# Performance work log

Hardware: AMD Instinct MI355X
Metric: run time of the kernel (lower is better)

Reference implementation:

```python
import jax, jax.numpy as jnp
import numpy as np

D_MODEL, D_STATE, D_CONV, EXPAND = 1024, 16, 4, 2
D_INNER = EXPAND * D_MODEL
B, L = 2, 4096
LN_EPS = 1e-5


def setup_inputs() -> dict:
    key = jax.random.key(0)
    ks = jax.random.split(key, 6)
    x = jax.random.normal(ks[0], (B, L, D_MODEL), dtype=jnp.float32)
    ln_gamma = jnp.ones((D_MODEL,), jnp.float32)
    ln_beta = jnp.zeros((D_MODEL,), jnp.float32)
    W_in = jax.random.normal(ks[1], (2 * D_INNER, D_MODEL), jnp.float32) / np.sqrt(D_MODEL).astype(np.float32)
    conv_w = jax.random.normal(ks[2], (D_INNER, 1, D_CONV), jnp.float32) * 0.1
    conv_b = jnp.zeros((D_INNER,), jnp.float32)
    W_out = jax.random.normal(ks[3], (D_MODEL, D_INNER), jnp.float32) / np.sqrt(D_INNER).astype(np.float32)
    A = jnp.eye(D_STATE, dtype=jnp.float32)
    Bm = jax.random.normal(ks[4], (D_STATE, D_INNER), jnp.float32) * 0.01
    Cm = jax.random.normal(ks[5], (D_STATE, D_INNER), jnp.float32) * 0.01
    return dict(x=x, ln_gamma=ln_gamma, ln_beta=ln_beta, W_in=W_in,
                conv_w=conv_w, conv_b=conv_b, W_out=W_out, A=A, Bm=Bm, Cm=Cm)


def _layernorm(x, gamma, beta):
    mu = jnp.mean(x, axis=-1, keepdims=True)
    var = jnp.mean(jnp.square(x - mu), axis=-1, keepdims=True)
    return (x - mu) * jax.lax.rsqrt(var + LN_EPS) * gamma + beta


def _causal_depthwise_conv(xp, conv_w, conv_b):
    # xp: (B, L, D_INNER) -> torch Conv1d(padding=K-1, groups=C) then slice [:L]
    # == left-pad K-1, valid depthwise conv.
    lhs = jnp.pad(xp.transpose(0, 2, 1), ((0, 0), (0, 0), (D_CONV - 1, 0)))  # (B,C,L+K-1)
    out = jax.lax.conv_general_dilated(
        lhs, conv_w, window_strides=(1,), padding='VALID',
        dimension_numbers=('NCH', 'OIH', 'NCH'), feature_group_count=D_INNER)
    return out.transpose(0, 2, 1) + conv_b  # (B, L, C)


def reference(x, ln_gamma, ln_beta, W_in, conv_w, conv_b, W_out, A, Bm, Cm):
    # scan permutation is identity (untrained optimizer state); masking disabled
    xn = _layernorm(x, ln_gamma, ln_beta)
    xz = jnp.einsum('bld,ed->ble', xn, W_in)          # (B, L, 2*D_INNER)
    x_part, z = jnp.split(xz, 2, axis=-1)             # each (B, L, D_INNER)
    x_conv = jax.nn.silu(_causal_depthwise_conv(x_part, conv_w, conv_b))

    # recurrence: s_t = s_{t-1} @ A.T + u_t @ B.T ; out_t = (x_conv_t + s_t @ C) * sigmoid(z_t)
    u_seq = x_part.transpose(1, 0, 2)                 # (L, B, D_INNER)
    xc_seq = x_conv.transpose(1, 0, 2)
    z_seq = z.transpose(1, 0, 2)

    def step(state, inp):
        u_t, xc_t, z_t = inp
        state = state @ A.T + u_t @ Bm.T              # (B, D_STATE)
        out = (xc_t + state @ Cm) * jax.nn.sigmoid(z_t)
        return state, out

    state0 = jnp.zeros((x.shape[0], D_STATE), x.dtype)
    _, ys = jax.lax.scan(step, state0, (u_seq, xc_seq, z_seq))
    y = ys.transpose(1, 0, 2)                         # (B, L, D_INNER)
    residual = jnp.einsum('bli,di->bld', y, W_out)    # (B, L, D_MODEL)
    return x + residual
```

## Files before the change

kernel.cpp:

```cpp
#include <hip/hip_runtime.h>
#include <hip/hip_bf16.h>
#include <math.h>

#define D_MODEL 1024
#define D_STATE 16
#define D_CONV 4
#define D_INNER 2048
#define BATCH 2
#define SEQ 4096
#define NROW (BATCH * SEQ)
#define LN_EPS 1e-5f

typedef __attribute__((ext_vector_type(8))) short  bf16x8_t;
typedef __attribute__((ext_vector_type(4))) float  f32x4_t;
typedef __attribute__((ext_vector_type(8))) unsigned short u16x8_t;

__device__ inline unsigned short f2bf(float f) {
    unsigned u = __float_as_uint(f);
    u += 0x7fffu + ((u >> 16) & 1u);
    return (unsigned short)(u >> 16);
}
__device__ inline float bf2f(unsigned short u) {
    return __uint_as_float((unsigned)u << 16);
}

#define GLL16(g, l)                                                            \
    __builtin_amdgcn_global_load_lds(                                          \
        (const __attribute__((address_space(1))) void*)(g),                    \
        (__attribute__((address_space(3))) void*)(l), 16, 0, 0)

#define FENCE asm volatile("" ::: "memory")
#define BAR do { FENCE; __builtin_amdgcn_s_barrier(); FENCE; } while (0)

__global__ __launch_bounds__(256) void cvt_all(const float* __restrict__ W_in,
                                               const float* __restrict__ W_out,
                                               const float* __restrict__ Bm,
                                               unsigned short* __restrict__ Win_bf,
                                               unsigned short* __restrict__ Wout_bf,
                                               unsigned short* __restrict__ Bm_bf) {
    const long long g = (long long)(blockIdx.x * 256 + threadIdx.x) * 8;
    const long long n1 = (long long)2 * D_INNER * D_MODEL;
    const long long n2 = n1 + (long long)D_MODEL * D_INNER;
    const float* src; unsigned short* dst; long long off;
    if (g < n1)      { src = W_in;  dst = Win_bf;  off = g; }
    else if (g < n2) { src = W_out; dst = Wout_bf; off = g - n1; }
    else             { src = Bm;    dst = Bm_bf;   off = g - n2; }
    const float4 a = *reinterpret_cast<const float4*>(src + off);
    const float4 b = *reinterpret_cast<const float4*>(src + off + 4);
    u16x8_t p;
    p[0] = f2bf(a.x); p[1] = f2bf(a.y); p[2] = f2bf(a.z); p[3] = f2bf(a.w);
    p[4] = f2bf(b.x); p[5] = f2bf(b.y); p[6] = f2bf(b.z); p[7] = f2bf(b.w);
    *reinterpret_cast<u16x8_t*>(dst + off) = p;
}

__global__ __launch_bounds__(256) void ln_kernel(const float* __restrict__ x,
                                                 const float* __restrict__ gamma,
                                                 const float* __restrict__ beta,
                                                 unsigned short* __restrict__ xn) {
    const int row = blockIdx.x;
    const int tid = threadIdx.x;
    const float4* xr = reinterpret_cast<const float4*>(x + (size_t)row * D_MODEL);
    float4 v = xr[tid];

    __shared__ float red[8];
    const int lane = tid & 63, wave = tid >> 6;

    float s = v.x + v.y + v.z + v.w;
    #pragma unroll
    for (int off = 32; off > 0; off >>= 1) s += __shfl_down(s, off, 64);
    if (lane == 0) red[wave] = s;
    __syncthreads();
    float mu = (red[0] + red[1] + red[2] + red[3]) * (1.0f / D_MODEL);
    __syncthreads();

    float dx = v.x - mu, dy = v.y - mu, dz = v.z - mu, dw = v.w - mu;
    float ss = dx * dx + dy * dy + dz * dz + dw * dw;
    #pragma unroll
    for (int off = 32; off > 0; off >>= 1) ss += __shfl_down(ss, off, 64);
    if (lane == 0) red[wave] = ss;
    __syncthreads();
    float var = (red[0] + red[1] + red[2] + red[3]) * (1.0f / D_MODEL);
    float rs = rsqrtf(var + LN_EPS);

    const float4 gv = reinterpret_cast<const float4*>(gamma)[tid];
    const float4 bv = reinterpret_cast<const float4*>(beta)[tid];
    ushort4 o;
    o.x = f2bf(dx * rs * gv.x + bv.x);
    o.y = f2bf(dy * rs * gv.y + bv.y);
    o.z = f2bf(dz * rs * gv.z + bv.z);
    o.w = f2bf(dw * rs * gv.w + bv.w);
    reinterpret_cast<ushort4*>(xn + (size_t)row * D_MODEL)[tid] = o;
}

__global__ __launch_bounds__(512) void gemm256_bf16(const short* __restrict__ A,
                                                    const short* __restrict__ B,
                                                    unsigned short* __restrict__ Cb,
                                                    int M, int N, int K) {
    __shared__ short lds[2 * 4 * 8192];

    const int tid = threadIdx.x;
    const int w = tid >> 6, l = tid & 63;
    const int row0 = blockIdx.y * 256;
    const int col0 = blockIdx.x * 256;
    const int wm = w >> 2;
    const int wn = w & 3;
    const int fr = l & 15;
    const int fc = (l >> 4) * 8;
    const int NT = K >> 6;

    const int qa = wm;
    const int qb = 2 + (wn >> 1);
    const int bb = (wn & 1) * 64;

    auto STAGE = [&](const short* __restrict__ G, int growbase, int k0,
                     int buf, int q) {
        #pragma unroll
        for (int j = 0; j < 2; ++j) {
            const int e = ((j * 8 + w) << 9) + l * 8;
            const int r = e >> 6;
            const int c = (e & 63) ^ ((r & 7) << 3);
            GLL16(G + (size_t)(growbase + r) * K + k0 + c,
                  &lds[buf * 32768 + q * 8192 + ((j * 8 + w) << 9)]);
        }
    };
    auto LDF = [&](int buf, int q, int r, int ks) -> bf16x8_t {
        const int c = (ks * 32 + fc) ^ ((r & 7) << 3);
        return *reinterpret_cast<const bf16x8_t*>(
            &lds[buf * 32768 + q * 8192 + r * 64 + c]);
    };

    f32x4_t acc[8][4] = {};
    bf16x8_t af[4][2], bA[2][2], bB[2][2];

#define MFMA_Q(mh, nh, bfr)                                                    \
    do {                                                                       \
        _Pragma("unroll")                                                      \
        for (int mi = 0; mi < 4; ++mi)                                         \
            _Pragma("unroll")                                                  \
            for (int ni = 0; ni < 2; ++ni)                                     \
                _Pragma("unroll")                                              \
                for (int ks = 0; ks < 2; ++ks)                                 \
                    acc[(mh) * 4 + mi][(nh) * 2 + ni] =                        \
                        __builtin_amdgcn_mfma_f32_16x16x32_bf16(               \
                            af[mi][ks], bfr[ni][ks],                           \
                            acc[(mh) * 4 + mi][(nh) * 2 + ni], 0, 0, 0);       \
    } while (0)

    STAGE(A, row0,       0, 0, 0);
    STAGE(A, row0 + 128, 0, 0, 1);
    STAGE(B, col0,       0, 0, 2);
    STAGE(B, col0 + 128, 0, 0, 3);
    if (NT > 1) {
        STAGE(B, col0,       64, 1, 2);
        STAGE(B, col0 + 128, 64, 1, 3);
        STAGE(A, row0,       64, 1, 0);
        asm volatile("s_waitcnt vmcnt(6)" ::: "memory");
    } else {
        asm volatile("s_waitcnt vmcnt(0)" ::: "memory");
    }
    BAR;

    for (int kt = 0; kt < NT; ++kt) {
        const int buf = kt & 1, nbuf = buf ^ 1;
        #pragma unroll
        for (int mi = 0; mi < 4; ++mi)
            #pragma unroll
            for (int ks = 0; ks < 2; ++ks)
                af[mi][ks] = LDF(buf, qa, mi * 16 + fr, ks);
        #pragma unroll
        for (int ni = 0; ni < 2; ++ni)
            #pragma unroll
            for (int ks = 0; ks < 2; ++ks)
                bA[ni][ks] = LDF(buf, qb, bb + ni * 16 + fr, ks);
        if (kt + 1 < NT) STAGE(A, row0 + 128, (kt + 1) << 6, nbuf, 1);
        BAR;
        __builtin_amdgcn_s_setprio(1);
        MFMA_Q(0, 0, bA);
        __builtin_amdgcn_s_setprio(0);
        BAR;
        #pragma unroll
        for (int ni = 0; ni < 2; ++ni)
            #pragma unroll
            for (int ks = 0; ks < 2; ++ks)
                bB[ni][ks] = LDF(buf, qb, bb + 32 + ni * 16 + fr, ks);
        BAR;
        __builtin_amdgcn_s_setprio(1);
        MFMA_Q(0, 1, bB);
        __builtin_amdgcn_s_setprio(0);
        BAR;
        #pragma unroll
        for (int mi = 0; mi < 4; ++mi)
            #pragma unroll
            for (int ks = 0; ks < 2; ++ks)
                af[mi][ks] = LDF(buf, qa, 64 + mi * 16 + fr, ks);
        if (kt + 2 < NT) {
            STAGE(B, col0,       (kt + 2) << 6, buf, 2);
            STAGE(B, col0 + 128, (kt + 2) << 6, buf, 3);
        }
        BAR;
        __builtin_amdgcn_s_setprio(1);
        MFMA_Q(1, 1, bB);
        __builtin_amdgcn_s_setprio(0);
        BAR;
        if (kt + 2 < NT) {
            STAGE(A, row0, (kt + 2) << 6, buf, 0);
            asm volatile("s_waitcnt vmcnt(6)" ::: "memory");
        } else {
            asm volatile("s_waitcnt vmcnt(0)" ::: "memory");
        }
        BAR;
        __builtin_amdgcn_s_setprio(1);
        MFMA_Q(1, 0, bA);
        __builtin_amdgcn_s_setprio(0);
        BAR;
    }
#undef MFMA_Q

    const int cr = (l >> 4) * 4;
    const int cc = l & 15;
    #pragma unroll
    for (int m = 0; m < 8; ++m) {
        #pragma unroll
        for (int n = 0; n < 4; ++n) {
            size_t base = (size_t)(row0 + wm * 128 + m * 16 + cr) * N +
                          (col0 + wn * 64 + n * 16 + cc);
            #pragma unroll
            for (int j = 0; j < 4; ++j)
                Cb[base + (size_t)j * N] = f2bf(acc[m][n][j]);
        }
    }
}

__global__ __launch_bounds__(512) void gemm_out(const short* __restrict__ A,
                                                const short* __restrict__ B,
                                                const float* __restrict__ add,
                                                float* __restrict__ C,
                                                int M, int N, int K) {
    __shared__ short lds[2 * 3 * 8192];

    const int tid = threadIdx.x;
    const int w = tid >> 6, l = tid & 63;

    const int id = blockIdx.y * gridDim.x + blockIdx.x;
    const int cpx = (gridDim.x * gridDim.y) >> 3;
    const int sid = (id & 7) * cpx + (id >> 3);
    const int row0 = (sid / gridDim.x) * 256;
    const int col0 = (sid % gridDim.x) * 128;

    const int wm = w >> 2;
    const int wn = w & 3;
    const int fr = l & 15;
    const int fc = (l >> 4) * 8;
    const int NT = K >> 6;
    const int bb = wn * 32;

    auto STAGE = [&](const short* __restrict__ G, int growbase, int k0,
                     int buf, int q) {
        #pragma unroll
        for (int j = 0; j < 2; ++j) {
            const int e = ((j * 8 + w) << 9) + l * 8;
            const int r = e >> 6;
            const int c = (e & 63) ^ ((r & 7) << 3);
            GLL16(G + (size_t)(growbase + r) * K + k0 + c,
                  &lds[buf * 24576 + q * 8192 + ((j * 8 + w) << 9)]);
        }
    };
    auto LDF = [&](int buf, int q, int r, int ks) -> bf16x8_t {
        const int c = (ks * 32 + fc) ^ ((r & 7) << 3);
        return *reinterpret_cast<const bf16x8_t*>(
            &lds[buf * 24576 + q * 8192 + r * 64 + c]);
    };

    f32x4_t acc[8][2] = {};
    bf16x8_t af[4][2], bA[2], bB[2];

#define MFMA_H(mh, an, bfr)                                                    \
    do {                                                                       \
        _Pragma("unroll")                                                      \
        for (int mi = 0; mi < 4; ++mi)                                         \
            _Pragma("unroll")                                                  \
            for (int ks = 0; ks < 2; ++ks)                                     \
                acc[(mh) * 4 + mi][(an)] =                                     \
                    __builtin_amdgcn_mfma_f32_16x16x32_bf16(                   \
                        af[mi][ks], bfr[ks], acc[(mh) * 4 + mi][(an)], 0, 0, 0);\
    } while (0)

    STAGE(A, row0,       0, 0, 0);
    STAGE(A, row0 + 128, 0, 0, 1);
    STAGE(B, col0,       0, 0, 2);
    if (NT > 1) {
        STAGE(B, col0, 64, 1, 2);
        STAGE(A, row0, 64, 1, 0);
        asm volatile("s_waitcnt vmcnt(4)" ::: "memory");
    } else {
        asm volatile("s_waitcnt vmcnt(0)" ::: "memory");
    }
    BAR;

    for (int kt = 0; kt < NT; ++kt) {
        const int buf = kt & 1, nbuf = buf ^ 1;
        #pragma unroll
        for (int mi = 0; mi < 4; ++mi)
            #pragma unroll
            for (int ks = 0; ks < 2; ++ks)
                af[mi][ks] = LDF(buf, wm, mi * 16 + fr, ks);
        #pragma unroll
        for (int ks = 0; ks < 2; ++ks)
            bA[ks] = LDF(buf, 2, bb + fr, ks);
        if (kt + 1 < NT) STAGE(A, row0 + 128, (kt + 1) << 6, nbuf, 1);
        BAR;
        __builtin_amdgcn_s_setprio(1);
        MFMA_H(0, 0, bA);
        __builtin_amdgcn_s_setprio(0);
        BAR;
        #pragma unroll
        for (int ks = 0; ks < 2; ++ks)
            bB[ks] = LDF(buf, 2, bb + 16 + fr, ks);
        BAR;
        __builtin_amdgcn_s_setprio(1);
        MFMA_H(0, 1, bB);
        __builtin_amdgcn_s_setprio(0);
        BAR;
        #pragma unroll
        for (int mi = 0; mi < 4; ++mi)
            #pragma unroll
            for (int ks = 0; ks < 2; ++ks)
                af[mi][ks] = LDF(buf, wm, 64 + mi * 16 + fr, ks);
        if (kt + 2 < NT) STAGE(B, col0, (kt + 2) << 6, buf, 2);
        BAR;
        __builtin_amdgcn_s_setprio(1);
        MFMA_H(1, 1, bB);
        __builtin_amdgcn_s_setprio(0);
        BAR;
        if (kt + 2 < NT) {
            STAGE(A, row0, (kt + 2) << 6, buf, 0);
            asm volatile("s_waitcnt vmcnt(4)" ::: "memory");
        } else {
            asm volatile("s_waitcnt vmcnt(0)" ::: "memory");
        }
        BAR;
        __builtin_amdgcn_s_setprio(1);
        MFMA_H(1, 0, bA);
        __builtin_amdgcn_s_setprio(0);
        BAR;
    }
#undef MFMA_H

    const int cr = (l >> 4) * 4;
    const int cc = l & 15;
    #pragma unroll
    for (int m = 0; m < 8; ++m) {
        #pragma unroll
        for (int n = 0; n < 2; ++n) {
            size_t base = (size_t)(row0 + wm * 128 + m * 16 + cr) * N +
                          (col0 + wn * 32 + n * 16 + cc);
            #pragma unroll
            for (int j = 0; j < 4; ++j)
                C[base + (size_t)j * N] = acc[m][n][j] + add[base + (size_t)j * N];
        }
    }
}

__global__ __launch_bounds__(64) void v_mfma(const unsigned short* __restrict__ xz,
                                             const unsigned short* __restrict__ Bmb,
                                             float* __restrict__ V) {
    const int l = threadIdx.x;
    const int r0 = blockIdx.x * 16;
    const int fr = l & 15;
    const int fk = (l >> 4) * 8;

    const unsigned short* aP = xz + (size_t)(r0 + fr) * (2 * D_INNER) + fk;
    const unsigned short* bP = Bmb + fr * D_INNER + fk;

    f32x4_t acc = {};
    #pragma unroll 4
    for (int k0 = 0; k0 < D_INNER; k0 += 32) {
        bf16x8_t a = *reinterpret_cast<const bf16x8_t*>(aP + k0);
        bf16x8_t b = *reinterpret_cast<const bf16x8_t*>(bP + k0);
        acc = __builtin_amdgcn_mfma_f32_16x16x32_bf16(a, b, acc, 0, 0, 0);
    }

    const int cr = (l >> 4) * 4;
    const int cc = l & 15;
    #pragma unroll
    for (int j = 0; j < 4; ++j)
        V[(size_t)(r0 + cr + j) * D_STATE + cc] = acc[j];
}

__global__ __launch_bounds__(256) void check_a(const float* __restrict__ A,
                                               int* __restrict__ flag) {
    const int i = threadIdx.x;
    if (i == 0) *flag = 0;
    __syncthreads();
    const float ex = ((i >> 4) == (i & 15)) ? 1.0f : 0.0f;
    unsigned long long bad = __ballot(A[i] != ex);
    if ((i & 63) == 0 && bad) atomicOr(flag, 1);
}

__global__ __launch_bounds__(256) void scan_par(const float* __restrict__ V,
                                                float* __restrict__ S,
                                                const int* __restrict__ flag) {
    if (*flag) return;
    const int p = blockIdx.x;
    const int b = p >> 4, s = p & 15;
    const int tid = threadIdx.x;
    const float* vb = V + (size_t)b * SEQ * D_STATE + s;
    float* sb = S + (size_t)b * SEQ * D_STATE + s;

    const int t0 = tid * 16;
    float v[16];
    float run = 0.0f;
    #pragma unroll
    for (int j = 0; j < 16; ++j) {
        run += vb[(size_t)(t0 + j) * D_STATE];
        v[j] = run;
    }

    const float tot = run;
    float sc = tot;
    #pragma unroll
    for (int off = 1; off < 64; off <<= 1) {
        float n = __shfl_up(sc, off, 64);
        if ((tid & 63) >= off) sc += n;
    }
    __shared__ float wtot[4];
    if ((tid & 63) == 63) wtot[tid >> 6] = sc;
    __syncthreads();
    float woff = 0.0f;
    #pragma unroll
    for (int w2 = 0; w2 < 4; ++w2)
        if (w2 < (tid >> 6)) woff += wtot[w2];
    const float excl = sc - tot + woff;

    #pragma unroll
    for (int j = 0; j < 16; ++j)
        sb[(size_t)(t0 + j) * D_STATE] = v[j] + excl;
}

#define SCAN_CHUNK 256

__global__ __launch_bounds__(64) void scan_seq(const float* __restrict__ V,
                                               const float* __restrict__ A,
                                               float* __restrict__ S,
                                               const int* __restrict__ flag) {
    if (*flag == 0) return;
    __shared__ float Al[D_STATE * D_STATE];
    __shared__ float Vl[2 * SCAN_CHUNK * D_STATE];
    __shared__ float Sl[2 * SCAN_CHUNK * D_STATE];

    const int tid = threadIdx.x;
    for (int i = tid; i < D_STATE * D_STATE; i += 64) Al[i] = A[i];
    __syncthreads();

    float st = 0.0f;
    const int bb = (tid >> 4) & 1;
    const int ss = tid & 15;

    for (int t0 = 0; t0 < SEQ; t0 += SCAN_CHUNK) {
        for (int idx = tid; idx < 2 * SCAN_CHUNK * D_STATE; idx += 64) {
            int b = idx >> 12;
            int rem = idx & 4095;
            Vl[idx] = V[((size_t)(b * SEQ + t0) * D_STATE) + rem];
        }
        __syncthreads();

        if (tid < 32) {
            float* vb = Vl + bb * SCAN_CHUNK * D_STATE + ss;
            float* sb = Sl + bb * SCAN_CHUNK * D_STATE + ss;
            for (int t = 0; t < SCAN_CHUNK; ++t) {
                float ns = vb[t * D_STATE];
                #pragma unroll
                for (int s2 = 0; s2 < D_STATE; ++s2) {
                    float other = __shfl(st, (tid & 16) | s2, 64);
                    ns = fmaf(Al[ss * D_STATE + s2], other, ns);
                }
                st = ns;
                sb[t * D_STATE] = st;
            }
        }
        __syncthreads();

        for (int idx = tid; idx < 2 * SCAN_CHUNK * D_STATE; idx += 64) {
            int b = idx >> 12;
            int rem = idx & 4095;
            S[((size_t)(b * SEQ + t0) * D_STATE) + rem] = Sl[idx];
        }
        __syncthreads();
    }
}

__global__ __launch_bounds__(256) void y_kernel(const unsigned short* __restrict__ xz,
                                                const float* __restrict__ S,
                                                const float* __restrict__ Cm,
                                                const float* __restrict__ convw,
                                                const float* __restrict__ convb,
                                                unsigned short* __restrict__ y) {
    const int tid = threadIdx.x;
    const int i0 = blockIdx.x * 512 + tid * 2;
    const int r0 = blockIdx.y * 64;
    const int tb0 = r0 & (SEQ - 1);

    const float4 w0 = *reinterpret_cast<const float4*>(&convw[i0 * D_CONV]);
    const float4 w1 = *reinterpret_cast<const float4*>(&convw[(i0 + 1) * D_CONV]);
    const float cb0 = convb[i0], cb1 = convb[i0 + 1];
    float cm0[D_STATE], cm1[D_STATE];
    #pragma unroll
    for (int s = 0; s < D_STATE; ++s) {
        float2 c = *reinterpret_cast<const float2*>(&Cm[s * D_INNER + i0]);
        cm0[s] = c.x; cm1[s] = c.y;
    }

    float2 xm1 = make_float2(0.f, 0.f), xm2 = xm1, xm3 = xm1;
    if (tb0 >= 1) { ushort2 u = *reinterpret_cast<const ushort2*>(&xz[(size_t)(r0 - 1) * (2 * D_INNER) + i0]); xm1 = make_float2(bf2f(u.x), bf2f(u.y)); }
    if (tb0 >= 2) { ushort2 u = *reinterpret_cast<const ushort2*>(&xz[(size_t)(r0 - 2) * (2 * D_INNER) + i0]); xm2 = make_float2(bf2f(u.x), bf2f(u.y)); }
    if (tb0 >= 3) { ushort2 u = *reinterpret_cast<const ushort2*>(&xz[(size_t)(r0 - 3) * (2 * D_INNER) + i0]); xm3 = make_float2(bf2f(u.x), bf2f(u.y)); }

    for (int r = r0; r < r0 + 64; ++r) {
        const ushort2 xu = *reinterpret_cast<const ushort2*>(&xz[(size_t)r * (2 * D_INNER) + i0]);
        const ushort2 zu = *reinterpret_cast<const ushort2*>(&xz[(size_t)r * (2 * D_INNER) + D_INNER + i0]);
        const float2 x0 = make_float2(bf2f(xu.x), bf2f(xu.y));

        float a0 = cb0;
        a0 = fmaf(w0.x, xm3.x, a0); a0 = fmaf(w0.y, xm2.x, a0);
        a0 = fmaf(w0.z, xm1.x, a0); a0 = fmaf(w0.w, x0.x, a0);
        float a1 = cb1;
        a1 = fmaf(w1.x, xm3.y, a1); a1 = fmaf(w1.y, xm2.y, a1);
        a1 = fmaf(w1.z, xm1.y, a1); a1 = fmaf(w1.w, x0.y, a1);

        const float xc0 = a0 / (1.0f + expf(-a0));
        const float xc1 = a1 / (1.0f + expf(-a1));

        const float4* Sp = reinterpret_cast<const float4*>(S + (size_t)r * D_STATE);
        const float4 s0 = Sp[0], s1 = Sp[1], s2 = Sp[2], s3 = Sp[3];
        const float sv[D_STATE] = {s0.x, s0.y, s0.z, s0.w, s1.x, s1.y, s1.z, s1.w,
                                   s2.x, s2.y, s2.z, s2.w, s3.x, s3.y, s3.z, s3.w};
        float sc0 = 0.f, sc1 = 0.f;
        #pragma unroll
        for (int s = 0; s < D_STATE; ++s) {
            sc0 = fmaf(sv[s], cm0[s], sc0);
            sc1 = fmaf(sv[s], cm1[s], sc1);
        }

        const float z0 = bf2f(zu.x), z1 = bf2f(zu.y);
        const float g0 = 1.0f / (1.0f + expf(-z0));
        const float g1 = 1.0f / (1.0f + expf(-z1));

        ushort2 o;
        o.x = f2bf((xc0 + sc0) * g0);
        o.y = f2bf((xc1 + sc1) * g1);
        *reinterpret_cast<ushort2*>(&y[(size_t)r * D_INNER + i0]) = o;

        xm3 = xm2; xm2 = xm1; xm1 = x0;
    }
}

extern "C" void kernel_launch(void* const* d_in, const int* in_sizes, int n_in,
                              void* d_out, int out_size, void* d_ws, size_t ws_size,
                              hipStream_t stream) {
    const float* x      = (const float*)d_in[0];
    const float* ln_g   = (const float*)d_in[1];
    const float* ln_b   = (const float*)d_in[2];
    const float* W_in   = (const float*)d_in[3];
    const float* conv_w = (const float*)d_in[4];
    const float* conv_b = (const float*)d_in[5];
    const float* W_out  = (const float*)d_in[6];
    const float* A      = (const float*)d_in[7];
    const float* Bm     = (const float*)d_in[8];
    const float* Cm     = (const float*)d_in[9];
    float* out = (float*)d_out;

    float* ws = (float*)d_ws;
    float* V  = ws;
    float* S  = V + (size_t)NROW * D_STATE;
    int*   flag = (int*)(S + (size_t)NROW * D_STATE);
    unsigned short* xz_bf  = (unsigned short*)(flag + 64);
    unsigned short* xn_bf  = xz_bf  + (size_t)NROW * 2 * D_INNER;
    unsigned short* Win_bf = xn_bf  + (size_t)NROW * D_MODEL;
    unsigned short* Wout_bf= Win_bf + (size_t)(2 * D_INNER) * D_MODEL;
    unsigned short* Bm_bf  = Wout_bf + (size_t)D_MODEL * D_INNER;
    unsigned short* y_bf   = Bm_bf  + (size_t)D_STATE * D_INNER;

    cvt_all<<<3088, 256, 0, stream>>>(W_in, W_out, Bm, Win_bf, Wout_bf, Bm_bf);

    ln_kernel<<<NROW, 256, 0, stream>>>(x, ln_g, ln_b, xn_bf);

    gemm256_bf16<<<dim3((2 * D_INNER) / 256, NROW / 256), 512, 0, stream>>>(
        (const short*)xn_bf, (const short*)Win_bf, xz_bf,
        NROW, 2 * D_INNER, D_MODEL);

    v_mfma<<<NROW / 16, 64, 0, stream>>>(xz_bf, Bm_bf, V);

    check_a<<<1, 256, 0, stream>>>(A, flag);
    scan_par<<<32, 256, 0, stream>>>(V, S, flag);
    scan_seq<<<1, 64, 0, stream>>>(V, A, S, flag);

    y_kernel<<<dim3(D_INNER / 512, NROW / 64), 256, 0, stream>>>(
        xz_bf, S, Cm, conv_w, conv_b, y_bf);

    gemm_out<<<dim3(D_MODEL / 128, NROW / 256), 512, 0, stream>>>(
        (const short*)y_bf, (const short*)Wout_bf, x, out,
        NROW, D_MODEL, D_INNER);
}
```

Before: 203.2 us.

## Prefetch next-tile fragments across k-steps and merge small launches

Measured after the change: 318.1 us. +56.5%, slower.

```diff
diff --git a/kernel.cpp b/kernel.cpp
--- a/kernel.cpp
+++ b/kernel.cpp
@@ -32,39 +32,40 @@
 #define FENCE asm volatile("" ::: "memory")
 #define BAR do { FENCE; __builtin_amdgcn_s_barrier(); FENCE; } while (0)
 
-__global__ __launch_bounds__(256) void cvt_all(const float* __restrict__ W_in,
-                                               const float* __restrict__ W_out,
-                                               const float* __restrict__ Bm,
-                                               unsigned short* __restrict__ Win_bf,
-                                               unsigned short* __restrict__ Wout_bf,
-                                               unsigned short* __restrict__ Bm_bf) {
-    const long long g = (long long)(blockIdx.x * 256 + threadIdx.x) * 8;
-    const long long n1 = (long long)2 * D_INNER * D_MODEL;
-    const long long n2 = n1 + (long long)D_MODEL * D_INNER;
-    const float* src; unsigned short* dst; long long off;
-    if (g < n1)      { src = W_in;  dst = Win_bf;  off = g; }
-    else if (g < n2) { src = W_out; dst = Wout_bf; off = g - n1; }
-    else             { src = Bm;    dst = Bm_bf;   off = g - n2; }
-    const float4 a = *reinterpret_cast<const float4*>(src + off);
-    const float4 b = *reinterpret_cast<const float4*>(src + off + 4);
-    u16x8_t p;
-    p[0] = f2bf(a.x); p[1] = f2bf(a.y); p[2] = f2bf(a.z); p[3] = f2bf(a.w);
-    p[4] = f2bf(b.x); p[5] = f2bf(b.y); p[6] = f2bf(b.z); p[7] = f2bf(b.w);
-    *reinterpret_cast<u16x8_t*>(dst + off) = p;
-}
-
-__global__ __launch_bounds__(256) void ln_kernel(const float* __restrict__ x,
-                                                 const float* __restrict__ gamma,
-                                                 const float* __restrict__ beta,
-                                                 unsigned short* __restrict__ xn) {
-    const int row = blockIdx.x;
+#define CVT_BLOCKS 3088
+__global__ __launch_bounds__(256) void pre_kernel(const float* __restrict__ x,
+                                                  const float* __restrict__ gamma,
+                                                  const float* __restrict__ beta,
+                                                  const float* __restrict__ W_in,
+                                                  const float* __restrict__ W_out,
+                                                  const float* __restrict__ Bm,
+                                                  unsigned short* __restrict__ xn,
+                                                  unsigned short* __restrict__ Win_bf,
+                                                  unsigned short* __restrict__ Wout_bf,
+                                                  unsigned short* __restrict__ Bm_bf) {
+    __shared__ float red[8];
     const int tid = threadIdx.x;
+    if (blockIdx.x < CVT_BLOCKS) {
+        const long long g = (long long)(blockIdx.x * 256 + tid) * 8;
+        const long long n1 = (long long)2 * D_INNER * D_MODEL;
+        const long long n2 = n1 + (long long)D_MODEL * D_INNER;
+        const float* src; unsigned short* dst; long long off;
+        if (g < n1)      { src = W_in;  dst = Win_bf;  off = g; }
+        else if (g < n2) { src = W_out; dst = Wout_bf; off = g - n1; }
+        else             { src = Bm;    dst = Bm_bf;   off = g - n2; }
+        const float4 a = *reinterpret_cast<const float4*>(src + off);
+        const float4 b = *reinterpret_cast<const float4*>(src + off + 4);
+        u16x8_t p;
+        p[0] = f2bf(a.x); p[1] = f2bf(a.y); p[2] = f2bf(a.z); p[3] = f2bf(a.w);
+        p[4] = f2bf(b.x); p[5] = f2bf(b.y); p[6] = f2bf(b.z); p[7] = f2bf(b.w);
+        *reinterpret_cast<u16x8_t*>(dst + off) = p;
+        return;
+    }
+    const int row = blockIdx.x - CVT_BLOCKS;
     const float4* xr = reinterpret_cast<const float4*>(x + (size_t)row * D_MODEL);
     float4 v = xr[tid];
 
-    __shared__ float red[8];
     const int lane = tid & 63, wave = tid >> 6;
-
     float s = v.x + v.y + v.z + v.w;
     #pragma unroll
     for (int off = 32; off > 0; off >>= 1) s += __shfl_down(s, off, 64);
@@ -130,9 +131,12 @@
     };
 
     f32x4_t acc[8][4] = {};
-    bf16x8_t af[4][2], bA[2][2], bB[2][2];
-
-#define MFMA_Q(mh, nh, bfr)                                                    \
+    bf16x8_t af[4][2];
+    bf16x8_t af2[4][2];
+    bf16x8_t bB[2][2];
+    bf16x8_t bA_e[2][2], bA_o[2][2];
+
+#define MFMA_Q(AF, mh, nh, BFR)                                                \
     do {                                                                       \
         _Pragma("unroll")                                                      \
         for (int mi = 0; mi < 4; ++mi)                                         \
@@ -142,9 +146,66 @@
                 for (int ks = 0; ks < 2; ++ks)                                 \
                     acc[(mh) * 4 + mi][(nh) * 2 + ni] =                        \
                         __builtin_amdgcn_mfma_f32_16x16x32_bf16(               \
-                            af[mi][ks], bfr[ni][ks],                           \
+                            AF[mi][ks], BFR[ni][ks],                           \
                             acc[(mh) * 4 + mi][(nh) * 2 + ni], 0, 0, 0);       \
     } while (0)
+
+    auto KT = [&](int kt, int buf, int nbuf,
+                  bf16x8_t (&bAc)[2][2], bf16x8_t (&bAn)[2][2]) {
+        if (kt + 1 < NT) STAGE(A, row0 + 128, (kt + 1) << 6, nbuf, 1);
+        BAR;
+        #pragma unroll
+        for (int ni = 0; ni < 2; ++ni)
+            #pragma unroll
+            for (int ks = 0; ks < 2; ++ks)
+                bB[ni][ks] = LDF(buf, qb, bb + 32 + ni * 16 + fr, ks);
+        __builtin_amdgcn_s_setprio(1);
+        MFMA_Q(af, 0, 0, bAc);
+        __builtin_amdgcn_s_setprio(0);
+        BAR;
+        BAR;
+        #pragma unroll
+        for (int mi = 0; mi < 4; ++mi)
+            #pragma unroll
+            for (int ks = 0; ks < 2; ++ks)
+                af2[mi][ks] = LDF(buf, qa, 64 + mi * 16 + fr, ks);
+        __builtin_amdgcn_s_setprio(1);
+        MFMA_Q(af, 0, 1, bB);
+        __builtin_amdgcn_s_setprio(0);
+        BAR;
+        if (kt + 2 < NT) {
+            STAGE(B, col0,       (kt + 2) << 6, buf, 2);
+            STAGE(B, col0 + 128, (kt + 2) << 6, buf, 3);
+        }
+        BAR;
+        __builtin_amdgcn_s_setprio(1);
+        MFMA_Q(af2, 1, 1, bB);
+        __builtin_amdgcn_s_setprio(0);
+        BAR;
+        if (kt + 2 < NT) {
+            STAGE(A, row0, (kt + 2) << 6, buf, 0);
+            asm volatile("s_waitcnt vmcnt(6)" ::: "memory");
+        } else {
+            asm volatile("s_waitcnt vmcnt(0)" ::: "memory");
+        }
+        BAR;
+        if (kt + 1 < NT) {
+            #pragma unroll
+            for (int mi = 0; mi < 4; ++mi)
+                #pragma unroll
+                for (int ks = 0; ks < 2; ++ks)
+                    af[mi][ks] = LDF(nbuf, qa, mi * 16 + fr, ks);
+            #pragma unroll
+            for (int ni = 0; ni < 2; ++ni)
+                #pragma unroll
+                for (int ks = 0; ks < 2; ++ks)
+                    bAn[ni][ks] = LDF(nbuf, qb, bb + ni * 16 + fr, ks);
+        }
+        __builtin_amdgcn_s_setprio(1);
+        MFMA_Q(af2, 1, 0, bAc);
+        __builtin_amdgcn_s_setprio(0);
+        BAR;
+    };
 
     STAGE(A, row0,       0, 0, 0);
     STAGE(A, row0 + 128, 0, 0, 1);
@@ -159,60 +220,20 @@
         asm volatile("s_waitcnt vmcnt(0)" ::: "memory");
     }
     BAR;
-
-    for (int kt = 0; kt < NT; ++kt) {
-        const int buf = kt & 1, nbuf = buf ^ 1;
-        #pragma unroll
-        for (int mi = 0; mi < 4; ++mi)
-            #pragma unroll
-            for (int ks = 0; ks < 2; ++ks)
-                af[mi][ks] = LDF(buf, qa, mi * 16 + fr, ks);
-        #pragma unroll
-        for (int ni = 0; ni < 2; ++ni)
-            #pragma unroll
-            for (int ks = 0; ks < 2; ++ks)
-                bA[ni][ks] = LDF(buf, qb, bb + ni * 16 + fr, ks);
-        if (kt + 1 < NT) STAGE(A, row0 + 128, (kt + 1) << 6, nbuf, 1);
-        BAR;
-        __builtin_amdgcn_s_setprio(1);
-        MFMA_Q(0, 0, bA);
-        __builtin_amdgcn_s_setprio(0);
-        BAR;
-        #pragma unroll
-        for (int ni = 0; ni < 2; ++ni)
-            #pragma unroll
-            for (int ks = 0; ks < 2; ++ks)
-                bB[ni][ks] = LDF(buf, qb, bb + 32 + ni * 16 + fr, ks);
-        BAR;
-        __builtin_amdgcn_s_setprio(1);
-        MFMA_Q(0, 1, bB);
-        __builtin_amdgcn_s_setprio(0);
-        BAR;
-        #pragma unroll
-        for (int mi = 0; mi < 4; ++mi)
-            #pragma unroll
-            for (int ks = 0; ks < 2; ++ks)
-                af[mi][ks] = LDF(buf, qa, 64 + mi * 16 + fr, ks);
-        if (kt + 2 < NT) {
-            STAGE(B, col0,       (kt + 2) << 6, buf, 2);
-            STAGE(B, col0 + 128, (kt + 2) << 6, buf, 3);
-        }
-        BAR;
-        __builtin_amdgcn_s_setprio(1);
-        MFMA_Q(1, 1, bB);
-        __builtin_amdgcn_s_setprio(0);
-        BAR;
-        if (kt + 2 < NT) {
-            STAGE(A, row0, (kt + 2) << 6, buf, 0);
-            asm volatile("s_waitcnt vmcnt(6)" ::: "memory");
-        } else {
-            asm volatile("s_waitcnt vmcnt(0)" ::: "memory");
-        }
-        BAR;
-        __builtin_amdgcn_s_setprio(1);
-        MFMA_Q(1, 0, bA);
-        __builtin_amdgcn_s_setprio(0);
-        BAR;
+    #pragma unroll
+    for (int mi = 0; mi < 4; ++mi)
+        #pragma unroll
+        for (int ks = 0; ks < 2; ++ks)
+            af[mi][ks] = LDF(0, qa, mi * 16 + fr, ks);
+    #pragma unroll
+    for (int ni = 0; ni < 2; ++ni)
+        #pragma unroll
+        for (int ks = 0; ks < 2; ++ks)
+            bA_e[ni][ks] = LDF(0, qb, bb + ni * 16 + fr, ks);
+
+    for (int kt = 0; kt < NT; kt += 2) {
+        KT(kt,     0, 1, bA_e, bA_o);
+        KT(kt + 1, 1, 0, bA_o, bA_e);
     }
 #undef MFMA_Q
 
@@ -272,9 +293,10 @@
     };
 
     f32x4_t acc[8][2] = {};
-    bf16x8_t af[4][2], bA[2], bB[2];
-
-#define MFMA_H(mh, an, bfr)                                                    \
+    bf16x8_t af[4][2], af2[4][2], bB[2];
+    bf16x8_t bA_e[2], bA_o[2];
+
+#define MFMA_H(AF, mh, an, BFR)                                                \
     do {                                                                       \
         _Pragma("unroll")                                                      \
         for (int mi = 0; mi < 4; ++mi)                                         \
@@ -282,8 +304,58 @@
             for (int ks = 0; ks < 2; ++ks)                                     \
                 acc[(mh) * 4 + mi][(an)] =                                     \
                     __builtin_amdgcn_mfma_f32_16x16x32_bf16(                   \
-                        af[mi][ks], bfr[ks], acc[(mh) * 4 + mi][(an)], 0, 0, 0);\
+                        AF[mi][ks], BFR[ks], acc[(mh) * 4 + mi][(an)], 0, 0, 0);\
     } while (0)
+
+    auto KT = [&](int kt, int buf, int nbuf,
+                  bf16x8_t (&bAc)[2], bf16x8_t (&bAn)[2]) {
+        if (kt + 1 < NT) STAGE(A, row0 + 128, (kt + 1) << 6, nbuf, 1);
+        BAR;
+        #pragma unroll
+        for (int ks = 0; ks < 2; ++ks)
+            bB[ks] = LDF(buf, 2, bb + 16 + fr, ks);
+        __builtin_amdgcn_s_setprio(1);
+        MFMA_H(af, 0, 0, bAc);
+        __builtin_amdgcn_s_setprio(0);
+        BAR;
+        BAR;
+        #pragma unroll
+        for (int mi = 0; mi < 4; ++mi)
+            #pragma unroll
+            for (int ks = 0; ks < 2; ++ks)
+                af2[mi][ks] = LDF(buf, wm, 64 + mi * 16 + fr, ks);
+        __builtin_amdgcn_s_setprio(1);
+        MFMA_H(af, 0, 1, bB);
+        __builtin_amdgcn_s_setprio(0);
+        BAR;
+        if (kt + 2 < NT) STAGE(B, col0, (kt + 2) << 6, buf, 2);
+        BAR;
+        __builtin_amdgcn_s_setprio(1);
+        MFMA_H(af2, 1, 1, bB);
+        __builtin_amdgcn_s_setprio(0);
+        BAR;
+        if (kt + 2 < NT) {
+            STAGE(A, row0, (kt + 2) << 6, buf, 0);
+            asm volatile("s_waitcnt vmcnt(4)" ::: "memory");
+        } else {
+            asm volatile("s_waitcnt vmcnt(0)" ::: "memory");
+        }
+        BAR;
+        if (kt + 1 < NT) {
+            #pragma unroll
+            for (int mi = 0; mi < 4; ++mi)
+                #pragma unroll
+                for (int ks = 0; ks < 2; ++ks)
+                    af[mi][ks] = LDF(nbuf, wm, mi * 16 + fr, ks);
+            #pragma unroll
+            for (int ks = 0; ks < 2; ++ks)
+                bAn[ks] = LDF(nbuf, 2, bb + fr, ks);
+        }
+        __builtin_amdgcn_s_setprio(1);
+        MFMA_H(af2, 1, 0, bAc);
+        __builtin_amdgcn_s_setprio(0);
+        BAR;
+    };
 
     STAGE(A, row0,       0, 0, 0);
     STAGE(A, row0 + 128, 0, 0, 1);
@@ -296,53 +368,18 @@
         asm volatile("s_waitcnt vmcnt(0)" ::: "memory");
     }
     BAR;
-
-    for (int kt = 0; kt < NT; ++kt) {
-        const int buf = kt & 1, nbuf = buf ^ 1;
-        #pragma unroll
-        for (int mi = 0; mi < 4; ++mi)
-            #pragma unroll
-            for (int ks = 0; ks < 2; ++ks)
-                af[mi][ks] = LDF(buf, wm, mi * 16 + fr, ks);
+    #pragma unroll
+    for (int mi = 0; mi < 4; ++mi)
         #pragma unroll
         for (int ks = 0; ks < 2; ++ks)
-            bA[ks] = LDF(buf, 2, bb + fr, ks);
-        if (kt + 1 < NT) STAGE(A, row0 + 128, (kt + 1) << 6, nbuf, 1);
-        BAR;
-        __builtin_amdgcn_s_setprio(1);
-        MFMA_H(0, 0, bA);
-        __builtin_amdgcn_s_setprio(0);
-        BAR;
-        #pragma unroll
-        for (int ks = 0; ks < 2; ++ks)
-            bB[ks] = LDF(buf, 2, bb + 16 + fr, ks);
-        BAR;
-        __builtin_amdgcn_s_setprio(1);
-        MFMA_H(0, 1, bB);
-        __builtin_amdgcn_s_setprio(0);
-        BAR;
-        #pragma unroll
-        for (int mi = 0; mi < 4; ++mi)
-            #pragma unroll
-            for (int ks = 0; ks < 2; ++ks)
-                af[mi][ks] = LDF(buf, wm, 64 + mi * 16 + fr, ks);
-        if (kt + 2 < NT) STAGE(B, col0, (kt + 2) << 6, buf, 2);
-        BAR;
-        __builtin_amdgcn_s_setprio(1);
-        MFMA_H(1, 1, bB);
-        __builtin_amdgcn_s_setprio(0);
-        BAR;
-        if (kt + 2 < NT) {
-            STAGE(A, row0, (kt + 2) << 6, buf, 0);
-            asm volatile("s_waitcnt vmcnt(4)" ::: "memory");
-        } else {
-            asm volatile("s_waitcnt vmcnt(0)" ::: "memory");
-        }
-        BAR;
-        __builtin_amdgcn_s_setprio(1);
-        MFMA_H(1, 0, bA);
-        __builtin_amdgcn_s_setprio(0);
-        BAR;
+            af[mi][ks] = LDF(0, wm, mi * 16 + fr, ks);
+    #pragma unroll
+    for (int ks = 0; ks < 2; ++ks)
+        bA_e[ks] = LDF(0, 2, bb + fr, ks);
+
+    for (int kt = 0; kt < NT; kt += 2) {
+        KT(kt,     0, 1, bA_e, bA_o);
+        KT(kt + 1, 1, 0, bA_o, bA_e);
     }
 #undef MFMA_H
 
@@ -387,23 +424,22 @@
         V[(size_t)(r0 + cr + j) * D_STATE + cc] = acc[j];
 }
 
-__global__ __launch_bounds__(256) void check_a(const float* __restrict__ A,
-                                               int* __restrict__ flag) {
-    const int i = threadIdx.x;
-    if (i == 0) *flag = 0;
+__global__ __launch_bounds__(256) void scan_par(const float* __restrict__ V,
+                                                const float* __restrict__ A,
+                                                float* __restrict__ S) {
+    __shared__ int nid;
+    const int tid = threadIdx.x;
+    if (tid == 0) nid = 0;
     __syncthreads();
-    const float ex = ((i >> 4) == (i & 15)) ? 1.0f : 0.0f;
-    unsigned long long bad = __ballot(A[i] != ex);
-    if ((i & 63) == 0 && bad) atomicOr(flag, 1);
-}
-
-__global__ __launch_bounds__(256) void scan_par(const float* __restrict__ V,
-                                                float* __restrict__ S,
-                                                const int* __restrict__ flag) {
-    if (*flag) return;
+    {
+        const float ex = ((tid >> 4) == (tid & 15)) ? 1.0f : 0.0f;
+        if (A[tid] != ex) atomicOr(&nid, 1);
+    }
+    __syncthreads();
+    if (nid) return;
+
     const int p = blockIdx.x;
     const int b = p >> 4, s = p & 15;
-    const int tid = threadIdx.x;
     const float* vb = V + (size_t)b * SEQ * D_STATE + s;
     float* sb = S + (size_t)b * SEQ * D_STATE + s;
 
@@ -441,14 +477,19 @@
 
 __global__ __launch_bounds__(64) void scan_seq(const float* __restrict__ V,
                                                const float* __restrict__ A,
-                                               float* __restrict__ S,
-                                               const int* __restrict__ flag) {
-    if (*flag == 0) return;
+                                               float* __restrict__ S) {
+    const int tid = threadIdx.x;
+    int bad = 0;
+    for (int i = tid; i < D_STATE * D_STATE; i += 64) {
+        const float ex = ((i >> 4) == (i & 15)) ? 1.0f : 0.0f;
+        if (A[i] != ex) bad = 1;
+    }
+    if (__ballot(bad) == 0ULL) return;
+
     __shared__ float Al[D_STATE * D_STATE];
     __shared__ float Vl[2 * SCAN_CHUNK * D_STATE];
     __shared__ float Sl[2 * SCAN_CHUNK * D_STATE];
 
-    const int tid = threadIdx.x;
     for (int i = tid; i < D_STATE * D_STATE; i += 64) Al[i] = A[i];
     __syncthreads();
 
@@ -572,17 +613,15 @@
     float* ws = (float*)d_ws;
     float* V  = ws;
     float* S  = V + (size_t)NROW * D_STATE;
-    int*   flag = (int*)(S + (size_t)NROW * D_STATE);
-    unsigned short* xz_bf  = (unsigned short*)(flag + 64);
+    unsigned short* xz_bf  = (unsigned short*)(S + (size_t)NROW * D_STATE);
     unsigned short* xn_bf  = xz_bf  + (size_t)NROW * 2 * D_INNER;
     unsigned short* Win_bf = xn_bf  + (size_t)NROW * D_MODEL;
     unsigned short* Wout_bf= Win_bf + (size_t)(2 * D_INNER) * D_MODEL;
     unsigned short* Bm_bf  = Wout_bf + (size_t)D_MODEL * D_INNER;
     unsigned short* y_bf   = Bm_bf  + (size_t)D_STATE * D_INNER;
 
-    cvt_all<<<3088, 256, 0, stream>>>(W_in, W_out, Bm, Win_bf, Wout_bf, Bm_bf);
-
-    ln_kernel<<<NROW, 256, 0, stream>>>(x, ln_g, ln_b, xn_bf);
+    pre_kernel<<<CVT_BLOCKS + NROW, 256, 0, stream>>>(
+        x, ln_g, ln_b, W_in, W_out, Bm, xn_bf, Win_bf, Wout_bf, Bm_bf);
 
     gemm256_bf16<<<dim3((2 * D_INNER) / 256, NROW / 256), 512, 0, stream>>>(
         (const short*)xn_bf, (const short*)Win_bf, xz_bf,
@@ -590,9 +629,8 @@
 
     v_mfma<<<NROW / 16, 64, 0, stream>>>(xz_bf, Bm_bf, V);
 
-    check_a<<<1, 256, 0, stream>>>(A, flag);
-    scan_par<<<32, 256, 0, stream>>>(V, S, flag);
-    scan_seq<<<1, 64, 0, stream>>>(V, A, S, flag);
+    scan_par<<<32, 256, 0, stream>>>(V, A, S);
+    scan_seq<<<1, 64, 0, stream>>>(V, A, S);
 
     y_kernel<<<dim3(D_INNER / 512, NROW / 64), 256, 0, stream>>>(
         xz_bf, S, Cm, conv_w, conv_b, y_bf);
```

## Precompute Bm·W_in projection, fuse prep kernels, and inline A-identity checks

Applied to the files above, without the earlier changes.

New measurement: 364.7 us. +79.5%, slower.

```diff
diff --git a/kernel.cpp b/kernel.cpp
--- a/kernel.cpp
+++ b/kernel.cpp
@@ -32,39 +32,50 @@
 #define FENCE asm volatile("" ::: "memory")
 #define BAR do { FENCE; __builtin_amdgcn_s_barrier(); FENCE; } while (0)
 
-__global__ __launch_bounds__(256) void cvt_all(const float* __restrict__ W_in,
-                                               const float* __restrict__ W_out,
-                                               const float* __restrict__ Bm,
-                                               unsigned short* __restrict__ Win_bf,
-                                               unsigned short* __restrict__ Wout_bf,
-                                               unsigned short* __restrict__ Bm_bf) {
-    const long long g = (long long)(blockIdx.x * 256 + threadIdx.x) * 8;
-    const long long n1 = (long long)2 * D_INNER * D_MODEL;
-    const long long n2 = n1 + (long long)D_MODEL * D_INNER;
-    const float* src; unsigned short* dst; long long off;
-    if (g < n1)      { src = W_in;  dst = Win_bf;  off = g; }
-    else if (g < n2) { src = W_out; dst = Wout_bf; off = g - n1; }
-    else             { src = Bm;    dst = Bm_bf;   off = g - n2; }
-    const float4 a = *reinterpret_cast<const float4*>(src + off);
-    const float4 b = *reinterpret_cast<const float4*>(src + off + 4);
-    u16x8_t p;
-    p[0] = f2bf(a.x); p[1] = f2bf(a.y); p[2] = f2bf(a.z); p[3] = f2bf(a.w);
-    p[4] = f2bf(b.x); p[5] = f2bf(b.y); p[6] = f2bf(b.z); p[7] = f2bf(b.w);
-    *reinterpret_cast<u16x8_t*>(dst + off) = p;
-}
-
-__global__ __launch_bounds__(256) void ln_kernel(const float* __restrict__ x,
-                                                 const float* __restrict__ gamma,
-                                                 const float* __restrict__ beta,
-                                                 unsigned short* __restrict__ xn) {
-    const int row = blockIdx.x;
+#define CVT_BLOCKS 3072
+__global__ __launch_bounds__(256) void pre_kernel(const float* __restrict__ x,
+                                                  const float* __restrict__ gamma,
+                                                  const float* __restrict__ beta,
+                                                  const float* __restrict__ W_in,
+                                                  const float* __restrict__ W_out,
+                                                  const float* __restrict__ Bm,
+                                                  unsigned short* __restrict__ xn,
+                                                  unsigned short* __restrict__ Win_bf,
+                                                  unsigned short* __restrict__ Wout_bf,
+                                                  unsigned short* __restrict__ Bmp_bf) {
+    __shared__ float red[8];
     const int tid = threadIdx.x;
+    if (blockIdx.x < CVT_BLOCKS) {
+        const long long g = (long long)(blockIdx.x * 256 + tid) * 8;
+        const long long n1 = (long long)2 * D_INNER * D_MODEL;
+        const float* src; unsigned short* dst; long long off;
+        if (g < n1) { src = W_in;  dst = Win_bf;  off = g; }
+        else        { src = W_out; dst = Wout_bf; off = g - n1; }
+        const float4 a = *reinterpret_cast<const float4*>(src + off);
+        const float4 b = *reinterpret_cast<const float4*>(src + off + 4);
+        u16x8_t p;
+        p[0] = f2bf(a.x); p[1] = f2bf(a.y); p[2] = f2bf(a.z); p[3] = f2bf(a.w);
+        p[4] = f2bf(b.x); p[5] = f2bf(b.y); p[6] = f2bf(b.z); p[7] = f2bf(b.w);
+        *reinterpret_cast<u16x8_t*>(dst + off) = p;
+        return;
+    }
+    if (blockIdx.x >= CVT_BLOCKS + NROW) {
+        const int flat = (blockIdx.x - CVT_BLOCKS - NROW) * 256 + tid;
+        const int d = flat & (D_MODEL - 1);
+        const int s = flat >> 10;
+        const float* bmr = Bm + (size_t)s * D_INNER;
+        float acc = 0.0f;
+        #pragma unroll 4
+        for (int e = 0; e < D_INNER; ++e)
+            acc = fmaf(bmr[e], W_in[(size_t)e * D_MODEL + d], acc);
+        Bmp_bf[(size_t)s * D_MODEL + d] = f2bf(acc);
+        return;
+    }
+    const int row = blockIdx.x - CVT_BLOCKS;
     const float4* xr = reinterpret_cast<const float4*>(x + (size_t)row * D_MODEL);
     float4 v = xr[tid];
 
-    __shared__ float red[8];
     const int lane = tid & 63, wave = tid >> 6;
-
     float s = v.x + v.y + v.z + v.w;
     #pragma unroll
     for (int off = 32; off > 0; off >>= 1) s += __shfl_down(s, off, 64);
@@ -361,20 +372,20 @@
     }
 }
 
-__global__ __launch_bounds__(64) void v_mfma(const unsigned short* __restrict__ xz,
-                                             const unsigned short* __restrict__ Bmb,
+__global__ __launch_bounds__(64) void v_mfma(const unsigned short* __restrict__ xn,
+                                             const unsigned short* __restrict__ Bmp,
                                              float* __restrict__ V) {
     const int l = threadIdx.x;
     const int r0 = blockIdx.x * 16;
     const int fr = l & 15;
     const int fk = (l >> 4) * 8;
 
-    const unsigned short* aP = xz + (size_t)(r0 + fr) * (2 * D_INNER) + fk;
-    const unsigned short* bP = Bmb + fr * D_INNER + fk;
+    const unsigned short* aP = xn + (size_t)(r0 + fr) * D_MODEL + fk;
+    const unsigned short* bP = Bmp + fr * D_MODEL + fk;
 
     f32x4_t acc = {};
     #pragma unroll 4
-    for (int k0 = 0; k0 < D_INNER; k0 += 32) {
+    for (int k0 = 0; k0 < D_MODEL; k0 += 32) {
         bf16x8_t a = *reinterpret_cast<const bf16x8_t*>(aP + k0);
         bf16x8_t b = *reinterpret_cast<const bf16x8_t*>(bP + k0);
         acc = __builtin_amdgcn_mfma_f32_16x16x32_bf16(a, b, acc, 0, 0, 0);
@@ -387,23 +398,22 @@
         V[(size_t)(r0 + cr + j) * D_STATE + cc] = acc[j];
 }
 
-__global__ __launch_bounds__(256) void check_a(const float* __restrict__ A,
-                                               int* __restrict__ flag) {
-    const int i = threadIdx.x;
-    if (i == 0) *flag = 0;
+__global__ __launch_bounds__(256) void scan_par(const float* __restrict__ V,
+                                                const float* __restrict__ A,
+                                                float* __restrict__ S) {
+    __shared__ int nid;
+    const int tid = threadIdx.x;
+    if (tid == 0) nid = 0;
     __syncthreads();
-    const float ex = ((i >> 4) == (i & 15)) ? 1.0f : 0.0f;
-    unsigned long long bad = __ballot(A[i] != ex);
-    if ((i & 63) == 0 && bad) atomicOr(flag, 1);
-}
-
-__global__ __launch_bounds__(256) void scan_par(const float* __restrict__ V,
-                                                float* __restrict__ S,
-                                                const int* __restrict__ flag) {
-    if (*flag) return;
+    {
+        const float ex = ((tid >> 4) == (tid & 15)) ? 1.0f : 0.0f;
+        if (A[tid] != ex) atomicOr(&nid, 1);
+    }
+    __syncthreads();
+    if (nid) return;
+
     const int p = blockIdx.x;
     const int b = p >> 4, s = p & 15;
-    const int tid = threadIdx.x;
     const float* vb = V + (size_t)b * SEQ * D_STATE + s;
     float* sb = S + (size_t)b * SEQ * D_STATE + s;
 
@@ -441,14 +451,19 @@
 
 __global__ __launch_bounds__(64) void scan_seq(const float* __restrict__ V,
                                                const float* __restrict__ A,
-                                               float* __restrict__ S,
-                                               const int* __restrict__ flag) {
-    if (*flag == 0) return;
+                                               float* __restrict__ S) {
+    const int tid = threadIdx.x;
+    int bad = 0;
+    for (int i = tid; i < D_STATE * D_STATE; i += 64) {
+        const float ex = ((i >> 4) == (i & 15)) ? 1.0f : 0.0f;
+        if (A[i] != ex) bad = 1;
+    }
+    if (__ballot(bad) == 0ULL) return;
+
     __shared__ float Al[D_STATE * D_STATE];
     __shared__ float Vl[2 * SCAN_CHUNK * D_STATE];
     __shared__ float Sl[2 * SCAN_CHUNK * D_STATE];
 
-    const int tid = threadIdx.x;
     for (int i = tid; i < D_STATE * D_STATE; i += 64) Al[i] = A[i];
     __syncthreads();
 
@@ -572,27 +587,24 @@
     float* ws = (float*)d_ws;
     float* V  = ws;
     float* S  = V + (size_t)NROW * D_STATE;
-    int*   flag = (int*)(S + (size_t)NROW * D_STATE);
-    unsigned short* xz_bf  = (unsigned short*)(flag + 64);
+    unsigned short* xz_bf  = (unsigned short*)(S + (size_t)NROW * D_STATE);
     unsigned short* xn_bf  = xz_bf  + (size_t)NROW * 2 * D_INNER;
     unsigned short* Win_bf = xn_bf  + (size_t)NROW * D_MODEL;
     unsigned short* Wout_bf= Win_bf + (size_t)(2 * D_INNER) * D_MODEL;
-    unsigned short* Bm_bf  = Wout_bf + (size_t)D_MODEL * D_INNER;
-    unsigned short* y_bf   = Bm_bf  + (size_t)D_STATE * D_INNER;
-
-    cvt_all<<<3088, 256, 0, stream>>>(W_in, W_out, Bm, Win_bf, Wout_bf, Bm_bf);
-
-    ln_kernel<<<NROW, 256, 0, stream>>>(x, ln_g, ln_b, xn_bf);
+    unsigned short* Bmp_bf = Wout_bf + (size_t)D_MODEL * D_INNER;
+    unsigned short* y_bf   = Bmp_bf + (size_t)D_STATE * D_MODEL;
+
+    pre_kernel<<<CVT_BLOCKS + NROW + 64, 256, 0, stream>>>(
+        x, ln_g, ln_b, W_in, W_out, Bm, xn_bf, Win_bf, Wout_bf, Bmp_bf);
 
     gemm256_bf16<<<dim3((2 * D_INNER) / 256, NROW / 256), 512, 0, stream>>>(
         (const short*)xn_bf, (const short*)Win_bf, xz_bf,
         NROW, 2 * D_INNER, D_MODEL);
 
-    v_mfma<<<NROW / 16, 64, 0, stream>>>(xz_bf, Bm_bf, V);
-
-    check_a<<<1, 256, 0, stream>>>(A, flag);
-    scan_par<<<32, 256, 0, stream>>>(V, S, flag);
-    scan_seq<<<1, 64, 0, stream>>>(V, A, S, flag);
+    v_mfma<<<NROW / 16, 64, 0, stream>>>(xn_bf, Bmp_bf, V);
+
+    scan_par<<<32, 256, 0, stream>>>(V, A, S);
+    scan_seq<<<1, 64, 0, stream>>>(V, A, S);
 
     y_kernel<<<dim3(D_INNER / 512, NROW / 64), 256, 0, stream>>>(
         xz_bf, S, Cm, conv_w, conv_b, y_bf);
```
